# Kernel tuning notes

Measured on AMD Instinct MI355X. Metric: run time of the kernel, lower is better.

Reference implementation:

```python
import jax, jax.numpy as jnp
import numpy as np

NUM_NODES = 100000
NUM_RELATIONS = 16
HIDDEN = 64
NUM_LAYERS = 3
NUM_EDGES = 1600000


def setup_inputs() -> dict:
    key = jax.random.key(0)
    ks = jax.random.split(key, 6)
    edge_index = jax.random.randint(ks[0], (2, NUM_EDGES), 0, NUM_NODES, dtype=jnp.int64 if jax.config.jax_enable_x64 else jnp.int32)
    edge_type = jax.random.randint(ks[1], (NUM_EDGES,), 0, NUM_RELATIONS, dtype=edge_index.dtype)
    scale = 1.0 / np.sqrt(HIDDEN)
    node_emb = jax.random.normal(ks[2], (NUM_NODES, HIDDEN), dtype=jnp.float32) * scale
    # Per-layer relation weights [L, R, d, h], root weights [L, d, h], bias [L, h]
    W = jax.random.normal(ks[3], (NUM_LAYERS, NUM_RELATIONS, HIDDEN, HIDDEN), dtype=jnp.float32) * scale
    W_root = jax.random.normal(ks[4], (NUM_LAYERS, HIDDEN, HIDDEN), dtype=jnp.float32) * scale
    bias = jnp.zeros((NUM_LAYERS, HIDDEN), dtype=jnp.float32)
    return {"edge_index": edge_index, "edge_type": edge_type,
            "node_emb": node_emb, "W": W, "W_root": W_root, "bias": bias}


def _rgcn_layer(x, src, dst, et, Wr, Wroot, b):
    # PyG RGCNConv: out_i = W_root x_i + b + sum_r (1/|N_r(i)|) sum_{j in N_r(i)} W_r x_j
    N, d = x.shape
    R = Wr.shape[0]
    # Transform all nodes by every relation weight: [R, N, h] (dense grouped GEMM)
    xW = jnp.einsum('nd,rdh->rnh', x, Wr)
    m = xW[et, src]                      # [E, h] per-edge messages (gather)
    seg = dst * R + et                   # joint (dst, relation) segment id
    counts = jax.ops.segment_sum(jnp.ones((m.shape[0],), dtype=x.dtype), seg, num_segments=N * R)
    norm = 1.0 / jnp.maximum(counts, 1.0)
    m = m * norm[seg][:, None]           # per-relation mean normalization
    agg = jax.ops.segment_sum(m, dst, num_segments=N)  # scatter-add over dst
    return agg + x @ Wroot + b


def reference(edge_index, edge_type, node_emb, W, W_root, bias):
    src, dst = edge_index[0], edge_index[1]
    x = node_emb  # note: Embedding.max_norm only applies on index lookups; .weight used raw here
    n_layers = W.shape[0]
    for i in range(n_layers):
        x = _rgcn_layer(x, src, dst, edge_type, W[i], W_root[i], bias[i])
        if i < n_layers - 1:
            x = jax.nn.relu(x)
    return x
```

## Files before the change

### kernel.cpp

```cpp
#include <hip/hip_runtime.h>


#define HID   64
#define NREL  16
#define KD    1088
#define NPB   16
#define NPW   2
#define LSTR  1096

#define NBKT  1024
#define BSH   7
#define BCAP  4096
#define FB    2048
#define CAPB  4096
#define CHA   8192

typedef __attribute__((ext_vector_type(8))) short bf16x8;
typedef __attribute__((ext_vector_type(4))) float f32x4;
typedef unsigned short us16;
typedef unsigned int u32;

__device__ __forceinline__ float b2f(us16 u) {
    union { u32 i; float f; } c; c.i = ((u32)u) << 16; return c.f;
}
__device__ __forceinline__ us16 f2b(float f) {
    union { float f; u32 i; } c; c.f = f;
    u32 x = c.i;
    return (us16)((x + 0x7FFFu + ((x >> 16) & 1u)) >> 16);
}


__global__ __launch_bounds__(256) void bucket_place(const int* __restrict__ ei,
                                                    const int* __restrict__ et,
                                                    int* __restrict__ cursor_b,
                                                    u32* __restrict__ packed, int E) {
    __shared__ int cnt[NBKT];
    __shared__ int bse[NBKT];
    const int t = threadIdx.x;
    for (int i = t; i < NBKT; i += 256) cnt[i] = 0;
    __syncthreads();
    const int* dstp = ei + E;
    int start = blockIdx.x * CHA, end = min(start + CHA, E);
    for (int e4 = start + t * 4; e4 < end; e4 += 1024) {
        if (e4 + 3 < end) {
            int4 d = *(const int4*)(dstp + e4);
            atomicAdd(&cnt[d.x >> BSH], 1);
            atomicAdd(&cnt[d.y >> BSH], 1);
            atomicAdd(&cnt[d.z >> BSH], 1);
            atomicAdd(&cnt[d.w >> BSH], 1);
        } else {
            for (int e = e4; e < end; ++e) atomicAdd(&cnt[dstp[e] >> BSH], 1);
        }
    }
    __syncthreads();
    for (int i = t; i < NBKT; i += 256) {
        int v = cnt[i];
        bse[i] = v ? (i * BCAP + atomicAdd(&cursor_b[i], v)) : 0;
        cnt[i] = 0;
    }
    __syncthreads();
    #define PLACE1(sv, dv, tv)                                            \
        { int b_ = (dv) >> BSH;                                           \
          int r_ = atomicAdd(&cnt[b_], 1);                                \
          packed[bse[b_] + r_] = (u32)(sv) | ((u32)(tv) << 17)            \
                               | ((u32)((dv) & 127) << 21); }
    for (int e4 = start + t * 4; e4 < end; e4 += 1024) {
        if (e4 + 3 < end) {
            int4 sv = *(const int4*)(ei + e4);
            int4 dv = *(const int4*)(dstp + e4);
            int4 tv = *(const int4*)(et + e4);
            PLACE1(sv.x, dv.x, tv.x);
            PLACE1(sv.y, dv.y, tv.y);
            PLACE1(sv.z, dv.z, tv.z);
            PLACE1(sv.w, dv.w, tv.w);
        } else {
            for (int e = e4; e < end; ++e) PLACE1(ei[e], dstp[e], et[e]);
        }
    }
    #undef PLACE1
}

__global__ __launch_bounds__(NBKT) void scan_buckets(const int* __restrict__ cursor_b,
                                                     int* __restrict__ bucket_base,
                                                     int* __restrict__ row_ptr,
                                                     int N, int E) {
    __shared__ int s[NBKT];
    int t = threadIdx.x;
    int v = cursor_b[t];
    s[t] = v; __syncthreads();
    for (int off = 1; off < NBKT; off <<= 1) {
        int tv = (t >= off) ? s[t - off] : 0;
        __syncthreads();
        s[t] += tv;
        __syncthreads();
    }
    int ex = s[t] - v;
    bucket_base[t] = ex;
    if (t == NBKT - 1) bucket_base[NBKT] = ex + v;
    if (t == 0) row_ptr[N] = E;
}

__global__ __launch_bounds__(256) void bucket_sort(const u32* __restrict__ packed,
                                                   const int* __restrict__ bucket_base,
                                                   u32* __restrict__ md,
                                                   int* __restrict__ row_ptr, int N) {
    __shared__ int hist[FB];
    __shared__ int ss[256];
    __shared__ u32 outb[CAPB];
    const int b = blockIdx.x, t = threadIdx.x;
    const int base = bucket_base[b];
    const int cnt = bucket_base[b + 1] - base;
    const u32* pk = packed + (size_t)b * BCAP;

    for (int i = t; i < FB; i += 256) hist[i] = 0;
    __syncthreads();
    for (int i = t; i < cnt; i += 256) {
        u32 p = pk[i];
        int f = (int)(((p >> 21) & 127u) * 16u + ((p >> 17) & 15u));
        atomicAdd(&hist[f], 1);
    }
    __syncthreads();
    int loc[8], s = 0;
    #pragma unroll
    for (int j = 0; j < 8; ++j) { loc[j] = hist[t * 8 + j]; s += loc[j]; }
    ss[t] = s; __syncthreads();
    for (int off = 1; off < 256; off <<= 1) {
        int tv = (t >= off) ? ss[t - off] : 0;
        __syncthreads();
        ss[t] += tv;
        __syncthreads();
    }
    int run = ss[t] - s;
    #pragma unroll
    for (int j = 0; j < 8; ++j) { hist[t * 8 + j] = run; run += loc[j]; }
    __syncthreads();
    if (t < 128) {
        int node = b * 128 + t;
        if (node < N) row_ptr[node] = base + hist[t * 16];
    }
    __syncthreads();
    for (int i = t; i < cnt; i += 256) {
        u32 p = pk[i];
        int f = (int)(((p >> 21) & 127u) * 16u + ((p >> 17) & 15u));
        int pos = atomicAdd(&hist[f], 1);
        u32 v = (p & 0x1FFFFu) | (((p >> 17) & 15u) << 20);
        if (pos < CAPB) outb[pos] = v;
        else            md[base + pos] = v;
    }
    __syncthreads();
    for (int i = t; i < cnt && i < CAPB; i += 256)
        md[base + i] = outb[i];
}

__global__ void convx_kernel(const float* __restrict__ x, us16* __restrict__ xb, int n4) {
    int i = blockIdx.x * 256 + threadIdx.x;
    if (i < n4) {
        float4 v = ((const float4*)x)[i];
        us16* o = xb + i * 4;
        o[0] = f2b(v.x); o[1] = f2b(v.y); o[2] = f2b(v.z); o[3] = f2b(v.w);
    }
}

__global__ void convw_kernel(const float* __restrict__ W, const float* __restrict__ Wroot,
                             us16* __restrict__ WcatT, int total, int L) {
    int i = blockIdx.x * 256 + threadIdx.x;
    if (i < total) {
        int l = i / (HID * KD);
        int rem = i % (HID * KD);
        int h = rem / KD, k = rem % KD;
        float v;
        if (k < NREL * HID) {
            int r = k >> 6, d = k & 63;
            v = W[(((size_t)l * NREL + r) * HID + d) * HID + h];
        } else {
            int d = k - NREL * HID;
            v = Wroot[((size_t)l * HID + d) * HID + h];
        }
        WcatT[i] = f2b(v);
    }
}


__device__ __forceinline__ void proc_window(
        u32 p_l, int c0, int wcnt, const us16* __restrict__ x_in, us16* Hrow, int lane,
        float& acc, int& runlen, int& prev, u32& mask)
{
    #pragma unroll 1
    for (int c = c0; c < wcnt; c += 16) {
        us16 hv[16]; int pe[16];
        #pragma unroll
        for (int j = 0; j < 16; ++j) {
            int idx = c + j; if (idx >= wcnt) idx = wcnt - 1;
            pe[j] = __builtin_amdgcn_readlane((int)p_l, idx);
            hv[j] = x_in[((u32)pe[j] & 0xFFFFFu) * HID + lane];
        }
        int m = wcnt - c; if (m > 16) m = 16;
        #pragma unroll
        for (int j = 0; j < 16; ++j) {
            if (j < m) {
                int r = (int)(((u32)pe[j]) >> 20);
                if (r != prev) {
                    if (prev >= 0) {
                        Hrow[(prev << 6) + lane] =
                            f2b(acc * __builtin_amdgcn_rcpf((float)runlen));
                        mask |= 1u << prev;
                    }
                    prev = r; acc = 0.f; runlen = 0;
                }
                acc += b2f(hv[j]); ++runlen;
            }
        }
    }
}

__global__ __launch_bounds__(512, 8) void layer_kernel(
        const us16* __restrict__ x_in,
        const int*  __restrict__ row_ptr,
        const u32*  __restrict__ md,
        const us16* __restrict__ WcatT,
        const float* __restrict__ bias,
        us16* __restrict__ x_out,
        float* __restrict__ out_f32,
        int flags, int N)
{
    __shared__ us16 H[NPB * LSTR];
    const int tid = threadIdx.x, wave = tid >> 6, lane = tid & 63;
    const int node0 = blockIdx.x * NPB;
    const int nodeq = node0 + wave * NPW;

    int rp[NPW + 1];
    #pragma unroll
    for (int i = 0; i <= NPW; ++i)
        rp[i] = __builtin_amdgcn_readfirstlane(row_ptr[min(nodeq + i, N)]);

    u32 pl[NPW]; us16 xr[NPW];
    #pragma unroll
    for (int q = 0; q < NPW; ++q) {
        int cnt = rp[q + 1] - rp[q];
        pl[q] = (lane < cnt) ? md[rp[q] + lane] : 0;
        xr[q] = (nodeq + q < N) ? x_in[(nodeq + q) * HID + lane] : (us16)0;
    }

    #pragma unroll
    for (int q = 0; q < NPW; ++q) {
        int node = nodeq + q;
        if (node >= N) break;
        int start = rp[q], cnt = rp[q + 1] - start;
        us16* Hrow = H + (wave * NPW + q) * LSTR;
        Hrow[NREL * HID + lane] = xr[q];

        float acc = 0.f;
        int runlen = 0, prev = -1;
        u32 mask = 0;

        proc_window(pl[q], 0, min(cnt, 64), x_in, Hrow, lane, acc, runlen, prev, mask);
        for (int w0 = 64; w0 < cnt; w0 += 64) {
            int wcnt = min(64, cnt - w0);
            u32 p2 = (lane < wcnt) ? md[start + w0 + lane] : 0;
            proc_window(p2, 0, wcnt, x_in, Hrow, lane, acc, runlen, prev, mask);
        }
        if (prev >= 0) {
            Hrow[(prev << 6) + lane] = f2b(acc * __builtin_amdgcn_rcpf((float)runlen));
            mask |= 1u << prev;
        }
        #pragma unroll
        for (int r = 0; r < NREL; ++r)
            if (!(mask & (1u << r))) Hrow[(r << 6) + lane] = 0;
    }
    __syncthreads();

    if (wave < 4) {
        const int n16 = lane & 15, quad = lane >> 4;
        f32x4 acc = {0.f, 0.f, 0.f, 0.f};
        const us16* Abase = H + n16 * LSTR + quad * 8;
        const us16* Bbase = WcatT + (size_t)(wave * 16 + n16) * KD + quad * 8;
        #pragma unroll 2
        for (int ks = 0; ks < KD / 32; ++ks) {
            bf16x8 af = *(const bf16x8*)(Abase + ks * 32);
            bf16x8 bf = *(const bf16x8*)(Bbase + ks * 32);
            acc = __builtin_amdgcn_mfma_f32_16x16x32_bf16(af, bf, acc, 0, 0, 0);
        }

        int col = wave * 16 + n16;
        float bv = bias[col];
        #pragma unroll
        for (int ri = 0; ri < 4; ++ri) {
            int nl = quad * 4 + ri, node = node0 + nl;
            if (node < N) {
                float v = acc[ri] + bv;
                if (flags & 1) v = fmaxf(v, 0.f);
                if (flags & 2) out_f32[node * HID + col] = v;
                else           x_out [node * HID + col] = f2b(v);
            }
        }
    }
}


extern "C" void kernel_launch(void* const* d_in, const int* in_sizes, int n_in,
                              void* d_out, int out_size, void* d_ws, size_t ws_size,
                              hipStream_t stream) {
    const int*   edge_index = (const int*)  d_in[0];
    const int*   edge_type  = (const int*)  d_in[1];
    const float* node_emb   = (const float*)d_in[2];
    const float* W          = (const float*)d_in[3];
    const float* Wroot      = (const float*)d_in[4];
    const float* bias       = (const float*)d_in[5];
    float* out = (float*)d_out;

    const int E = in_sizes[1];
    const int N = in_sizes[2] / HID;
    const int L = in_sizes[5] / HID;

    char* p = (char*)d_ws;
    size_t off = 0;
    auto carve = [&](size_t bytes) {
        void* q = p + off;
        off = (off + bytes + 255) & ~(size_t)255;
        return q;
    };
    int*   cursor_b    = (int*)  carve((size_t)NBKT * 4);
    int*   bucket_base = (int*)  carve((size_t)(NBKT + 1) * 4);
    int*   row_ptr     = (int*)  carve((size_t)(N + 1) * 4);
    u32*   packed      = (u32*)  carve((size_t)NBKT * BCAP * 4);
    u32*   md          = (u32*)  carve((size_t)E * 4);
    us16*  xb0         = (us16*) carve((size_t)N * HID * 2);
    us16*  xb1         = (us16*) carve((size_t)N * HID * 2);
    us16*  WcatT       = (us16*) carve((size_t)L * HID * KD * 2);
    (void)ws_size; (void)n_in; (void)out_size;

    hipMemsetAsync(cursor_b, 0, (size_t)NBKT * 4, stream);

    const int nblkA = (E + CHA - 1) / CHA;
    bucket_place<<<nblkA, 256, 0, stream>>>(edge_index, edge_type, cursor_b, packed, E);
    scan_buckets<<<1, NBKT, 0, stream>>>(cursor_b, bucket_base, row_ptr, N, E);
    bucket_sort<<<(N + 127) / 128, 256, 0, stream>>>(packed, bucket_base, md, row_ptr, N);

    convx_kernel<<<(N * HID / 4 + 255) / 256, 256, 0, stream>>>(node_emb, xb0, N * HID / 4);
    int wtot = L * HID * KD;
    convw_kernel<<<(wtot + 255) / 256, 256, 0, stream>>>(W, Wroot, WcatT, wtot, L);

    int gl = (N + NPB - 1) / NPB;
    us16* xin = xb0;
    us16* xother = xb1;
    for (int l = 0; l < L; ++l) {
        int last = (l == L - 1);
        int flags = (last ? 2 : 1);
        layer_kernel<<<gl, 512, 0, stream>>>(
            xin, row_ptr, md,
            WcatT + (size_t)l * HID * KD, bias + (size_t)l * HID,
            last ? nullptr : xother, last ? out : nullptr,
            flags, N);
        us16* t = xin; xin = xother; xother = t;
    }
}
```

Before: 526.2 us.

## Stage neighbor row gathers through LDS with 16-byte global_load_lds

Replaces the per-lane 2-byte gathers of neighbor feature rows with wide 16-byte direct global-to-LDS loads: each lane fetches a 16-byte chunk of one of 16 neighbor rows (indices distributed via ds_bpermute), then reads the values back from a per-wave LDS staging buffer. This cuts the number of memory instructions and makes each access wide, but it waits on vmcnt(0) every 16 edges, which serializes latency. It also adds 16KB of shared memory per block and lowers the launch-bounds occupancy hint from 8 to 6.

```diff
diff --git a/kernel.cpp b/kernel.cpp
--- a/kernel.cpp
+++ b/kernel.cpp
@@ -27,6 +27,12 @@
     union { float f; u32 i; } c; c.f = f;
     u32 x = c.i;
     return (us16)((x + 0x7FFFu + ((x >> 16) & 1u)) >> 16);
+}
+
+__device__ __forceinline__ void gl_lds16(const us16* g, us16* l) {
+    __builtin_amdgcn_global_load_lds(
+        (const __attribute__((address_space(1))) void*)g,
+        (__attribute__((address_space(3))) void*)l, 16, 0, 0);
 }
 
 
@@ -182,19 +188,32 @@
 
 
 __device__ __forceinline__ void proc_window(
-        u32 p_l, int c0, int wcnt, const us16* __restrict__ x_in, us16* Hrow, int lane,
-        float& acc, int& runlen, int& prev, u32& mask)
+        u32 p_l, int wcnt, const us16* __restrict__ x_in, us16* Hrow, us16* stage,
+        int lane, float& acc, int& runlen, int& prev, u32& mask)
 {
     #pragma unroll 1
-    for (int c = c0; c < wcnt; c += 16) {
-        us16 hv[16]; int pe[16];
+    for (int c = 0; c < wcnt; c += 16) {
+        int last = wcnt - 1;
+        int i0 = c + (lane >> 3);     if (i0 > last) i0 = last;
+        int i1 = c + 8 + (lane >> 3); if (i1 > last) i1 = last;
+        u32 m0 = (u32)__builtin_amdgcn_ds_bpermute(i0 << 2, (int)p_l);
+        u32 m1 = (u32)__builtin_amdgcn_ds_bpermute(i1 << 2, (int)p_l);
+        asm volatile("s_waitcnt lgkmcnt(0)" ::: "memory");
+        const us16* g0 = x_in + (size_t)(m0 & 0xFFFFFu) * HID + (lane & 7) * 8;
+        const us16* g1 = x_in + (size_t)(m1 & 0xFFFFFu) * HID + (lane & 7) * 8;
+        gl_lds16(g0, stage);
+        gl_lds16(g1, stage + 512);
+        asm volatile("s_waitcnt vmcnt(0)" ::: "memory");
+        __builtin_amdgcn_sched_barrier(0);
+
+        int m = wcnt - c; if (m > 16) m = 16;
+        int pe[16]; us16 hv[16];
         #pragma unroll
         for (int j = 0; j < 16; ++j) {
-            int idx = c + j; if (idx >= wcnt) idx = wcnt - 1;
+            int idx = c + j; if (idx > last) idx = last;
             pe[j] = __builtin_amdgcn_readlane((int)p_l, idx);
-            hv[j] = x_in[((u32)pe[j] & 0xFFFFFu) * HID + lane];
-        }
-        int m = wcnt - c; if (m > 16) m = 16;
+            hv[j] = stage[j * 64 + lane];
+        }
         #pragma unroll
         for (int j = 0; j < 16; ++j) {
             if (j < m) {
@@ -213,7 +232,7 @@
     }
 }
 
-__global__ __launch_bounds__(512, 8) void layer_kernel(
+__global__ __launch_bounds__(512, 6) void layer_kernel(
         const us16* __restrict__ x_in,
         const int*  __restrict__ row_ptr,
         const u32*  __restrict__ md,
@@ -224,9 +243,11 @@
         int flags, int N)
 {
     __shared__ us16 H[NPB * LSTR];
+    __shared__ us16 SB[8 * 1024];
     const int tid = threadIdx.x, wave = tid >> 6, lane = tid & 63;
     const int node0 = blockIdx.x * NPB;
     const int nodeq = node0 + wave * NPW;
+    us16* stage = SB + wave * 1024;
 
     int rp[NPW + 1];
     #pragma unroll
@@ -253,11 +274,13 @@
         int runlen = 0, prev = -1;
         u32 mask = 0;
 
-        proc_window(pl[q], 0, min(cnt, 64), x_in, Hrow, lane, acc, runlen, prev, mask);
+        proc_window(pl[q], min(cnt, 64), x_in, Hrow, stage, lane,
+                    acc, runlen, prev, mask);
         for (int w0 = 64; w0 < cnt; w0 += 64) {
             int wcnt = min(64, cnt - w0);
             u32 p2 = (lane < wcnt) ? md[start + w0 + lane] : 0;
-            proc_window(p2, 0, wcnt, x_in, Hrow, lane, acc, runlen, prev, mask);
+            proc_window(p2, wcnt, x_in, Hrow, stage, lane,
+                        acc, runlen, prev, mask);
         }
         if (prev >= 0) {
             Hrow[(prev << 6) + lane] = f2b(acc * __builtin_amdgcn_rcpf((float)runlen));
```

Result: slower. 573.9 us (+9.1%).
